# Kernel optimization log

Hardware: AMD Instinct MI355X
Metric: run time of the kernel (lower is better)

The kernel has to match this reference:

```python
import jax, jax.numpy as jnp
import numpy as np

def setup_inputs() -> dict:
    key = jax.random.key(0)
    k1, k2, k3, k4 = jax.random.split(key, 4)
    B, S, D = 256, 1024, 512
    story = jax.random.normal(k1, (B, S, D), dtype=jnp.float32)
    query = jax.random.normal(k2, (B, D), dtype=jnp.float32)
    # Wa_1 = nn.Linear(512, 1): weight [1,512], bias [1]
    Wa_w = jax.random.normal(k3, (D,), dtype=jnp.float32) * (1.0 / np.sqrt(D))
    Wa_b = jax.random.normal(k4, (1,), dtype=jnp.float32) * 0.01
    return {"story": story, "query": query, "Wa_w": Wa_w, "Wa_b": Wa_b}

def reference(story, query, Wa_w, Wa_b):
    # story: [B,S,D], query: [B,D] -> broadcast add + tanh
    atten_emb = jnp.tanh(story + query[:, None, :])          # [B,S,D]
    # dropout is identity in eval mode (training=False)
    scores = jnp.einsum('bsd,d->bs', atten_emb, Wa_w) + Wa_b  # [B,S]
    w = jax.nn.softmax(scores, axis=1)                        # [B,S]
    out = jnp.einsum('bs,bsd->bd', w, story)                  # [B,D]
    return out
```

## Files before the change

### kernel.cpp

```cpp
#include <hip/hip_runtime.h>
#include <math.h>

#define BB 256
#define SS 1024
#define DD 512
#define CC 8
#define ROWS_PER_BLOCK (SS / CC)
#define WAVES_PER_BLOCK 4
#define ROWS_PER_WAVE (ROWS_PER_BLOCK / WAVES_PER_BLOCK)

typedef float f4 __attribute__((ext_vector_type(4)));

__device__ __forceinline__ f4 ldnt(const float* p) {
    return __builtin_nontemporal_load((const f4*)p);
}

__device__ __forceinline__ float fast_tanh(float x) {
    return 1.0f - 2.0f / (__expf(2.0f * x) + 1.0f);
}

__device__ __forceinline__ float dot_tanh(f4 v, f4 q, f4 w) {
    return fast_tanh(v.x + q.x) * w.x + fast_tanh(v.y + q.y) * w.y +
           fast_tanh(v.z + q.z) * w.z + fast_tanh(v.w + q.w) * w.w;
}

__global__ __launch_bounds__(256, 4) void memn2n_partial(
    const float* __restrict__ story, const float* __restrict__ query,
    const float* __restrict__ Wa_w,
    float* __restrict__ wsO, float* __restrict__ wsL)
{
    const int g = blockIdx.x;
    const int b = g / CC;
    const int c = g % CC;
    const int lane = threadIdx.x & 63;
    const int wave = threadIdx.x >> 6;

    const int d0 = lane * 4;
    const int d1 = 256 + lane * 4;

    const f4 q0 = *(const f4*)(query + (size_t)b * DD + d0);
    const f4 q1 = *(const f4*)(query + (size_t)b * DD + d1);
    const f4 w0 = *(const f4*)(Wa_w + d0);
    const f4 w1 = *(const f4*)(Wa_w + d1);

    const int sBeg = c * ROWS_PER_BLOCK + wave * ROWS_PER_WAVE;
    const float* rowp = story + ((size_t)b * SS + sBeg) * DD;

    float l = 0.0f;
    f4 a0 = (f4)0.0f;
    f4 a1 = (f4)0.0f;

    f4 n0a = ldnt(rowp + d0);
    f4 n0b = ldnt(rowp + d1);
    f4 n1a = ldnt(rowp + DD + d0);
    f4 n1b = ldnt(rowp + DD + d1);

    for (int it = 0; it < ROWS_PER_WAVE / 2; ++it) {
        const f4 c0a = n0a, c0b = n0b, c1a = n1a, c1b = n1b;
        const float* np = rowp + 2 * DD;
        if (it + 1 < ROWS_PER_WAVE / 2) {
            n0a = ldnt(np + d0);
            n0b = ldnt(np + d1);
            n1a = ldnt(np + DD + d0);
            n1b = ldnt(np + DD + d1);
        }
        rowp = np;

        float p0 = dot_tanh(c0a, q0, w0) + dot_tanh(c0b, q1, w1);
        float p1 = dot_tanh(c1a, q0, w0) + dot_tanh(c1b, q1, w1);

        const float t0 = __shfl_xor(p0, 32, 64);
        const float t1 = __shfl_xor(p1, 32, 64);
        float s = (lane < 32) ? (p0 + t0) : (p1 + t1);
        s += __shfl_xor(s, 16, 64);
        s += __shfl_xor(s, 8, 64);
        s += __shfl_xor(s, 4, 64);
        s += __shfl_xor(s, 2, 64);
        s += __shfl_xor(s, 1, 64);
        const float o = __shfl_xor(s, 32, 64);
        const float pe0 = __expf((lane < 32) ? s : o);
        const float pe1 = __expf((lane < 32) ? o : s);

        l += pe0 + pe1;
        a0 += pe0 * c0a + pe1 * c1a;
        a1 += pe0 * c0b + pe1 * c1b;
    }

    __shared__ float ll[WAVES_PER_BLOCK];
    __shared__ float lo[WAVES_PER_BLOCK][DD];

    *(f4*)(&lo[wave][d0]) = a0;
    *(f4*)(&lo[wave][d1]) = a1;
    if (lane == 0) ll[wave] = l;
    __syncthreads();

    const int t = threadIdx.x;
    const float s0 = lo[0][t] + lo[1][t] + lo[2][t] + lo[3][t];
    const float s1 = lo[0][t + 256] + lo[1][t + 256] + lo[2][t + 256] + lo[3][t + 256];
    wsO[(size_t)g * DD + t] = s0;
    wsO[(size_t)g * DD + t + 256] = s1;
    if (t == 0)
        wsL[g] = ll[0] + ll[1] + ll[2] + ll[3];
}

__global__ __launch_bounds__(128) void memn2n_combine(
    const float* __restrict__ wsO, const float* __restrict__ wsL,
    float* __restrict__ out)
{
    const int b = blockIdx.x;
    const int t = threadIdx.x;

    float L = 0.0f;
#pragma unroll
    for (int c = 0; c < CC; ++c)
        L += wsL[b * CC + c];
    const float inv = 1.0f / L;

    const int d = t * 4;
    f4 acc = (f4)0.0f;
#pragma unroll
    for (int c = 0; c < CC; ++c)
        acc += *(const f4*)(wsO + ((size_t)(b * CC + c)) * DD + d);
    acc *= inv;
    *(f4*)(out + (size_t)b * DD + d) = acc;
}

extern "C" void kernel_launch(void* const* d_in, const int* in_sizes, int n_in,
                              void* d_out, int out_size, void* d_ws, size_t ws_size,
                              hipStream_t stream) {
    const float* story = (const float*)d_in[0];
    const float* query = (const float*)d_in[1];
    const float* Wa_w  = (const float*)d_in[2];
    float* out = (float*)d_out;

    float* wsO = (float*)d_ws;
    float* wsL = wsO + (size_t)BB * CC * DD;

    memn2n_partial<<<BB * CC, 256, 0, stream>>>(story, query, Wa_w, wsO, wsL);
    memn2n_combine<<<BB, 128, 0, stream>>>(wsO, wsL, out);
}
```

Before: 662.6 us.

## Fuse combine into partial kernel via last-block atomic counter; cheaper tanh math

Replaces the separate combine kernel with a last-block-done pattern: each block bumps a per-batch atomic counter, and the final block for that batch reduces the partial outputs and writes the result. The tanh/score computation is also restructured around exp2 and the hardware reciprocal, with constants folded so each element costs fewer instructions. This removes one kernel launch and cuts ALU work, but adds a memset launch, fences and atomics. The faster approximations can slightly change numerical accuracy.

```diff
diff --git a/kernel.cpp b/kernel.cpp
--- a/kernel.cpp
+++ b/kernel.cpp
@@ -15,19 +15,32 @@
     return __builtin_nontemporal_load((const f4*)p);
 }
 
-__device__ __forceinline__ float fast_tanh(float x) {
-    return 1.0f - 2.0f / (__expf(2.0f * x) + 1.0f);
+__device__ __forceinline__ float rcp_fast(float x) {
+    return __builtin_amdgcn_rcpf(x);
 }
 
-__device__ __forceinline__ float dot_tanh(f4 v, f4 q, f4 w) {
-    return fast_tanh(v.x + q.x) * w.x + fast_tanh(v.y + q.y) * w.y +
-           fast_tanh(v.z + q.z) * w.z + fast_tanh(v.w + q.w) * w.w;
+#if __has_builtin(__builtin_amdgcn_exp2f)
+__device__ __forceinline__ float exp2_fast(float x) { return __builtin_amdgcn_exp2f(x); }
+#else
+__device__ __forceinline__ float exp2_fast(float x) { return __expf(x * 0.69314718056f); }
+#endif
+
+#define K2E 2.8853900817779268f
+#define L2E 1.4426950408889634f
+
+__device__ __forceinline__ float neg_acc(f4 v, f4 qk, f4 w2, float acc) {
+    acc = fmaf(w2.x, rcp_fast(exp2_fast(fmaf(v.x, K2E, qk.x)) + 1.0f), acc);
+    acc = fmaf(w2.y, rcp_fast(exp2_fast(fmaf(v.y, K2E, qk.y)) + 1.0f), acc);
+    acc = fmaf(w2.z, rcp_fast(exp2_fast(fmaf(v.z, K2E, qk.z)) + 1.0f), acc);
+    acc = fmaf(w2.w, rcp_fast(exp2_fast(fmaf(v.w, K2E, qk.w)) + 1.0f), acc);
+    return acc;
 }
 
-__global__ __launch_bounds__(256, 4) void memn2n_partial(
+__global__ __launch_bounds__(256, 4) void memn2n_fused(
     const float* __restrict__ story, const float* __restrict__ query,
     const float* __restrict__ Wa_w,
-    float* __restrict__ wsO, float* __restrict__ wsL)
+    float* __restrict__ wsO, float* __restrict__ wsL, int* __restrict__ cnt,
+    float* __restrict__ out)
 {
     const int g = blockIdx.x;
     const int b = g / CC;
@@ -42,6 +55,9 @@
     const f4 q1 = *(const f4*)(query + (size_t)b * DD + d1);
     const f4 w0 = *(const f4*)(Wa_w + d0);
     const f4 w1 = *(const f4*)(Wa_w + d1);
+    const f4 qk0 = q0 * K2E, qk1 = q1 * K2E;
+    const f4 w20 = w0 * 2.0f, w21 = w1 * 2.0f;
+    const float Sw = w0.x + w0.y + w0.z + w0.w + w1.x + w1.y + w1.z + w1.w;
 
     const int sBeg = c * ROWS_PER_BLOCK + wave * ROWS_PER_WAVE;
     const float* rowp = story + ((size_t)b * SS + sBeg) * DD;
@@ -66,8 +82,8 @@
         }
         rowp = np;
 
-        float p0 = dot_tanh(c0a, q0, w0) + dot_tanh(c0b, q1, w1);
-        float p1 = dot_tanh(c1a, q0, w0) + dot_tanh(c1b, q1, w1);
+        float p0 = Sw - neg_acc(c0b, qk1, w21, neg_acc(c0a, qk0, w20, 0.0f));
+        float p1 = Sw - neg_acc(c1b, qk1, w21, neg_acc(c1a, qk0, w20, 0.0f));
 
         const float t0 = __shfl_xor(p0, 32, 64);
         const float t1 = __shfl_xor(p1, 32, 64);
@@ -78,8 +94,8 @@
         s += __shfl_xor(s, 2, 64);
         s += __shfl_xor(s, 1, 64);
         const float o = __shfl_xor(s, 32, 64);
-        const float pe0 = __expf((lane < 32) ? s : o);
-        const float pe1 = __expf((lane < 32) ? o : s);
+        const float pe0 = exp2_fast(((lane < 32) ? s : o) * L2E);
+        const float pe1 = exp2_fast(((lane < 32) ? o : s) * L2E);
 
         l += pe0 + pe1;
         a0 += pe0 * c0a + pe1 * c1a;
@@ -88,6 +104,7 @@
 
     __shared__ float ll[WAVES_PER_BLOCK];
     __shared__ float lo[WAVES_PER_BLOCK][DD];
+    __shared__ int lastFlag;
 
     *(f4*)(&lo[wave][d0]) = a0;
     *(f4*)(&lo[wave][d1]) = a1;
@@ -101,28 +118,35 @@
     wsO[(size_t)g * DD + t + 256] = s1;
     if (t == 0)
         wsL[g] = ll[0] + ll[1] + ll[2] + ll[3];
-}
 
-__global__ __launch_bounds__(128) void memn2n_combine(
-    const float* __restrict__ wsO, const float* __restrict__ wsL,
-    float* __restrict__ out)
-{
-    const int b = blockIdx.x;
-    const int t = threadIdx.x;
+    __syncthreads();
+    if (t == 0) {
+        __threadfence();
+        const int old = __hip_atomic_fetch_add(&cnt[b], 1, __ATOMIC_ACQ_REL,
+                                               __HIP_MEMORY_SCOPE_AGENT);
+        lastFlag = (old == CC - 1);
+    }
+    __syncthreads();
+    if (!lastFlag) return;
 
     float L = 0.0f;
 #pragma unroll
-    for (int c = 0; c < CC; ++c)
-        L += wsL[b * CC + c];
-    const float inv = 1.0f / L;
+    for (int cc = 0; cc < CC; ++cc)
+        L += __hip_atomic_load(&wsL[b * CC + cc], __ATOMIC_RELAXED,
+                               __HIP_MEMORY_SCOPE_AGENT);
+    const float inv = rcp_fast(L);
 
-    const int d = t * 4;
-    f4 acc = (f4)0.0f;
+    float acc0 = 0.0f, acc1 = 0.0f;
 #pragma unroll
-    for (int c = 0; c < CC; ++c)
-        acc += *(const f4*)(wsO + ((size_t)(b * CC + c)) * DD + d);
-    acc *= inv;
-    *(f4*)(out + (size_t)b * DD + d) = acc;
+    for (int cc = 0; cc < CC; ++cc) {
+        const float* base = wsO + (size_t)(b * CC + cc) * DD;
+        acc0 += __hip_atomic_load(base + t, __ATOMIC_RELAXED,
+                                  __HIP_MEMORY_SCOPE_AGENT);
+        acc1 += __hip_atomic_load(base + t + 256, __ATOMIC_RELAXED,
+                                  __HIP_MEMORY_SCOPE_AGENT);
+    }
+    out[(size_t)b * DD + t] = acc0 * inv;
+    out[(size_t)b * DD + t + 256] = acc1 * inv;
 }
 
 extern "C" void kernel_launch(void* const* d_in, const int* in_sizes, int n_in,
@@ -135,7 +159,9 @@
 
     float* wsO = (float*)d_ws;
     float* wsL = wsO + (size_t)BB * CC * DD;
+    int*   cnt = (int*)(wsL + (size_t)BB * CC);
 
-    memn2n_partial<<<BB * CC, 256, 0, stream>>>(story, query, Wa_w, wsO, wsL);
-    memn2n_combine<<<BB, 128, 0, stream>>>(wsO, wsL, out);
+    hipMemsetAsync(cnt, 0, BB * sizeof(int), stream);
+    memn2n_fused<<<BB * CC, 256, 0, stream>>>(story, query, Wa_w,
+                                              wsO, wsL, cnt, out);
 }
```

Measured after the change: 860.1 us. 1.3x slower.
